# Kernel tuning notes

Measured on AMD Instinct MI355X. Metric: run time of the kernel, lower is better.

## Reference

```python
import jax, jax.numpy as jnp
import numpy as np

D = 512
H_G = 8
H_L = 8
WIN = 2
B = 4
S = 2048
LN_EPS = 1e-5


def layer_norm(x, g, b):
    m = jnp.mean(x, axis=-1, keepdims=True)
    v = jnp.mean(jnp.square(x - m), axis=-1, keepdims=True)
    return (x - m) * jax.lax.rsqrt(v + LN_EPS) * g + b


def mha(x, w_in, b_in, w_out, b_out, n_heads, mask=None):
    # x: [B', S', D]; w_in: [3D, D]; torch nn.MultiheadAttention math (eval, no dropout)
    Bp, Sp, Dm = x.shape
    dh = Dm // n_heads
    qkv = x @ w_in.T + b_in                      # [B', S', 3D]
    q, k, v = jnp.split(qkv, 3, axis=-1)
    sp = lambda t: t.reshape(Bp, Sp, n_heads, dh).transpose(0, 2, 1, 3)
    q, k, v = sp(q), sp(k), sp(v)                # [B', H, S', dh]
    scale = 1.0 / np.sqrt(dh).astype(np.float32)
    scores = jnp.einsum('bhqd,bhkd->bhqk', q, k) * scale
    if mask is not None:
        scores = scores + mask
    attn = jax.nn.softmax(scores, axis=-1)
    out = jnp.einsum('bhqk,bhkd->bhqd', attn, v)
    out = out.transpose(0, 2, 1, 3).reshape(Bp, Sp, Dm)
    return out @ w_out.T + b_out


def setup_inputs() -> dict:
    key = jax.random.key(0)
    ks = jax.random.split(key, 12)
    s = 0.02
    inp = {
        'x': jax.random.normal(ks[0], (B, S, D), jnp.float32),
        'ln1_g': jnp.ones((D,), jnp.float32), 'ln1_b': jnp.zeros((D,), jnp.float32),
        'ln2_g': jnp.ones((D,), jnp.float32), 'ln2_b': jnp.zeros((D,), jnp.float32),
        'ln3_g': jnp.ones((D,), jnp.float32), 'ln3_b': jnp.zeros((D,), jnp.float32),
        'gw_in': jax.random.normal(ks[1], (3 * D, D), jnp.float32) * s,
        'gb_in': jnp.zeros((3 * D,), jnp.float32),
        'gw_out': jax.random.normal(ks[2], (D, D), jnp.float32) * s,
        'gb_out': jnp.zeros((D,), jnp.float32),
        'lw_in': jax.random.normal(ks[3], (3 * D, D), jnp.float32) * s,
        'lb_in': jnp.zeros((3 * D,), jnp.float32),
        'lw_out': jax.random.normal(ks[4], (D, D), jnp.float32) * s,
        'lb_out': jnp.zeros((D,), jnp.float32),
        'gate_w': jax.random.normal(ks[5], (D, D), jnp.float32) * s,
        'gate_b': jnp.zeros((D,), jnp.float32),
        'ff_w1': jax.random.normal(ks[6], (4 * D, D), jnp.float32) * s,
        'ff_b1': jnp.zeros((4 * D,), jnp.float32),
        'ff_w2': jax.random.normal(ks[7], (D, 4 * D), jnp.float32) * s,
        'ff_b2': jnp.zeros((D,), jnp.float32),
    }
    return inp


def reference(x, ln1_g, ln1_b, ln2_g, ln2_b, ln3_g, ln3_b,
              gw_in, gb_in, gw_out, gb_out,
              lw_in, lb_in, lw_out, lb_out,
              gate_w, gate_b, ff_w1, ff_b1, ff_w2, ff_b2):
    Bb, Ss, Dm = x.shape
    x_norm = layer_norm(x, ln1_g, ln1_b)

    # global causal attention
    causal = jnp.triu(jnp.full((Ss, Ss), -jnp.inf, jnp.float32), 1)
    g_out = mha(x_norm, gw_in, gb_in, gw_out, gb_out, H_G, mask=causal)

    xl = x_norm.reshape(Bb * (Ss // WIN), WIN, Dm)
    l_out = mha(xl, lw_in, lb_in, lw_out, lb_out, H_L).reshape(Bb, Ss, Dm)

    gate = jax.nn.sigmoid(x_norm @ gate_w.T + gate_b)
    x = x + gate * g_out + (1.0 - gate) * l_out

    h = layer_norm(x, ln2_g, ln2_b)
    h = jax.nn.gelu(h @ ff_w1.T + ff_b1, approximate=False) @ ff_w2.T + ff_b2
    x = x + h
    return layer_norm(x, ln3_g, ln3_b)
```

## Files before the change

### kernel.cpp

```cpp
#include <hip/hip_runtime.h>
#include <math.h>
#include <stdint.h>

typedef unsigned short u16;
typedef __attribute__((ext_vector_type(4))) unsigned short u16x4;
typedef __attribute__((ext_vector_type(8))) unsigned short u16x8;
typedef __attribute__((ext_vector_type(8))) short s16x8;
typedef __attribute__((ext_vector_type(4))) float f32x4;

constexpr int Bc = 4;
constexpr int Sq = 2048;
constexpr int Dm = 512;
constexpr int Mrows = Bc * Sq;
constexpr int QW = 3072;

__device__ inline float b2f(u16 h) {
  union { uint32_t u; float f; } x; x.u = (uint32_t)h << 16; return x.f;
}
__device__ inline u16 f2bf(float f) {
  union { float f; uint32_t u; } x; x.f = f;
  uint32_t r = (x.u + 0x7fffu + ((x.u >> 16) & 1u)) >> 16;
  return (u16)r;
}

constexpr size_t W_GWIN  = 0;
constexpr size_t W_LWIN  = 786432;
constexpr size_t W_GWOUT = 1572864;
constexpr size_t W_LWOUT = 1835008;
constexpr size_t W_GATE  = 2097152;
constexpr size_t W_FF1   = 2359296;
constexpr size_t W_FF2   = 3407872;
constexpr size_t W_TOTAL = 4456448;

__global__ __launch_bounds__(256) void wconv_kernel(
    const float* __restrict__ gw_in, const float* __restrict__ lw_in,
    const float* __restrict__ gw_out, const float* __restrict__ lw_out,
    const float* __restrict__ gate_w, const float* __restrict__ ff_w1,
    const float* __restrict__ ff_w2, u16* __restrict__ dst) {
  size_t idx = ((size_t)blockIdx.x * 256 + threadIdx.x) * 4;
  if (idx >= W_TOTAL) return;
  const float* src; size_t base;
  if      (idx < W_LWIN)  { src = gw_in;  base = W_GWIN;  }
  else if (idx < W_GWOUT) { src = lw_in;  base = W_LWIN;  }
  else if (idx < W_LWOUT) { src = gw_out; base = W_GWOUT; }
  else if (idx < W_GATE)  { src = lw_out; base = W_LWOUT; }
  else if (idx < W_FF1)   { src = gate_w; base = W_GATE;  }
  else if (idx < W_FF2)   { src = ff_w1;  base = W_FF1;   }
  else                    { src = ff_w2;  base = W_FF2;   }
  float4 v = *reinterpret_cast<const float4*>(src + (idx - base));
  u16x4 o = { f2bf(v.x), f2bf(v.y), f2bf(v.z), f2bf(v.w) };
  *reinterpret_cast<u16x4*>(dst + idx) = o;
}

template <bool OB>
__global__ __launch_bounds__(128) void ln_kernel(
    const float* __restrict__ in, const float* __restrict__ add,
    const float* __restrict__ add2,
    const float* __restrict__ g, const float* __restrict__ b,
    void* __restrict__ outp) {
  const int row = blockIdx.x;
  const int t = threadIdx.x;
  float4 v = reinterpret_cast<const float4*>(in + (size_t)row * Dm)[t];
  if (add != nullptr) {
    float4 a = reinterpret_cast<const float4*>(add + (size_t)row * Dm)[t];
    v.x += a.x; v.y += a.y; v.z += a.z; v.w += a.w;
  }
  if (add2 != nullptr) {
    float4 a = reinterpret_cast<const float4*>(add2 + (size_t)row * Dm)[t];
    v.x += a.x; v.y += a.y; v.z += a.z; v.w += a.w;
  }
  float s  = v.x + v.y + v.z + v.w;
  float s2 = v.x*v.x + v.y*v.y + v.z*v.z + v.w*v.w;
  #pragma unroll
  for (int o = 32; o > 0; o >>= 1) {
    s  += __shfl_down(s, o);
    s2 += __shfl_down(s2, o);
  }
  __shared__ float rs[2], rs2[2];
  if ((t & 63) == 0) { rs[t >> 6] = s; rs2[t >> 6] = s2; }
  __syncthreads();
  const float mean = (rs[0] + rs[1]) * (1.0f / Dm);
  const float var  = (rs2[0] + rs2[1]) * (1.0f / Dm) - mean * mean;
  const float rstd = rsqrtf(var + 1e-5f);
  float4 gv = reinterpret_cast<const float4*>(g)[t];
  float4 bv = reinterpret_cast<const float4*>(b)[t];
  float ox = (v.x - mean) * rstd * gv.x + bv.x;
  float oy = (v.y - mean) * rstd * gv.y + bv.y;
  float oz = (v.z - mean) * rstd * gv.z + bv.z;
  float ow = (v.w - mean) * rstd * gv.w + bv.w;
  if (OB) {
    u16x4 o4 = { f2bf(ox), f2bf(oy), f2bf(oz), f2bf(ow) };
    *reinterpret_cast<u16x4*>((u16*)outp + (size_t)row * Dm + t * 4) = o4;
  } else {
    float4 o4; o4.x = ox; o4.y = oy; o4.z = oz; o4.w = ow;
    reinterpret_cast<float4*>((float*)outp + (size_t)row * Dm)[t] = o4;
  }
}

template <int ACT, bool OUT_BF16>
__global__ __launch_bounds__(256) void mfma_gemm(
    const u16* __restrict__ A, const u16* __restrict__ W,
    const float* __restrict__ bias, const float* __restrict__ bias2, int bsplit,
    void* __restrict__ Cout, int N, int K) {
  __shared__ u16 sA[128 * 32];
  __shared__ u16 sW[128 * 32];
  const int tid  = threadIdx.x;
  const int wid  = tid >> 6, lane = tid & 63;
  const int lr   = lane & 15, kh = lane >> 4;
  const int wm   = wid >> 1, wn = wid & 1;
  const int m0   = blockIdx.y * 128, n0 = blockIdx.x * 128;
  const int row0 = tid >> 2,        ko0 = (tid & 3) * 8;
  const int row1 = (256 + tid) >> 2, ko1 = (tid & 3) * 8;

  f32x4 acc[4][4] = {};
  for (int k0 = 0; k0 < K; k0 += 32) {
    __syncthreads();
    __builtin_amdgcn_global_load_lds(
        (const __attribute__((address_space(1))) void*)(A + (size_t)(m0 + row0) * K + k0 + ko0),
        (__attribute__((address_space(3))) void*)(sA + wid * 512), 16, 0, 0);
    __builtin_amdgcn_global_load_lds(
        (const __attribute__((address_space(1))) void*)(A + (size_t)(m0 + row1) * K + k0 + ko1),
        (__attribute__((address_space(3))) void*)(sA + 2048 + wid * 512), 16, 0, 0);
    __builtin_amdgcn_global_load_lds(
        (const __attribute__((address_space(1))) void*)(W + (size_t)(n0 + row0) * K + k0 + ko0),
        (__attribute__((address_space(3))) void*)(sW + wid * 512), 16, 0, 0);
    __builtin_amdgcn_global_load_lds(
        (const __attribute__((address_space(1))) void*)(W + (size_t)(n0 + row1) * K + k0 + ko1),
        (__attribute__((address_space(3))) void*)(sW + 2048 + wid * 512), 16, 0, 0);
    __syncthreads();
    s16x8 af[4], bf[4];
    #pragma unroll
    for (int mf = 0; mf < 4; ++mf)
      af[mf] = *reinterpret_cast<const s16x8*>(&sA[(wm * 64 + mf * 16 + lr) * 32 + kh * 8]);
    #pragma unroll
    for (int nf = 0; nf < 4; ++nf)
      bf[nf] = *reinterpret_cast<const s16x8*>(&sW[(wn * 64 + nf * 16 + lr) * 32 + kh * 8]);
    #pragma unroll
    for (int mf = 0; mf < 4; ++mf)
      #pragma unroll
      for (int nf = 0; nf < 4; ++nf)
        acc[mf][nf] = __builtin_amdgcn_mfma_f32_16x16x32_bf16(af[mf], bf[nf], acc[mf][nf], 0, 0, 0);
  }
  #pragma unroll
  for (int nf = 0; nf < 4; ++nf) {
    const int col = n0 + wn * 64 + nf * 16 + lr;
    const float bv = (bias2 != nullptr && col >= bsplit) ? bias2[col - bsplit] : bias[col];
    #pragma unroll
    for (int mf = 0; mf < 4; ++mf) {
      #pragma unroll
      for (int j = 0; j < 4; ++j) {
        const int rowg = m0 + wm * 64 + mf * 16 + kh * 4 + j;
        float v = acc[mf][nf][j] + bv;
        if (ACT == 1) v = 1.0f / (1.0f + expf(-v));
        else if (ACT == 2) v = 0.5f * v * (1.0f + erff(v * 0.70710678118654752440f));
        if (OUT_BF16) ((u16*)Cout)[(size_t)rowg * N + col] = f2bf(v);
        else          ((float*)Cout)[(size_t)rowg * N + col] = v;
      }
    }
  }
}

__global__ __launch_bounds__(256) void mfma_gemm_sk(
    const u16* __restrict__ A, const u16* __restrict__ W,
    const float* __restrict__ bias, float* __restrict__ C0, float* __restrict__ C1,
    int N, int Kt) {
  __shared__ u16 sA[128 * 32];
  __shared__ u16 sW[128 * 32];
  const int tid  = threadIdx.x;
  const int wid  = tid >> 6, lane = tid & 63;
  const int lr   = lane & 15, kh = lane >> 4;
  const int wm   = wid >> 1, wn = wid & 1;
  const int m0   = blockIdx.y * 128, n0 = blockIdx.x * 128;
  const int z    = blockIdx.z;
  const int kbeg = z * (Kt / 2), kend = kbeg + (Kt / 2);
  const int row0 = tid >> 2,        ko0 = (tid & 3) * 8;
  const int row1 = (256 + tid) >> 2, ko1 = (tid & 3) * 8;

  f32x4 acc[4][4] = {};
  for (int k0 = kbeg; k0 < kend; k0 += 32) {
    __syncthreads();
    __builtin_amdgcn_global_load_lds(
        (const __attribute__((address_space(1))) void*)(A + (size_t)(m0 + row0) * Kt + k0 + ko0),
        (__attribute__((address_space(3))) void*)(sA + wid * 512), 16, 0, 0);
    __builtin_amdgcn_global_load_lds(
        (const __attribute__((address_space(1))) void*)(A + (size_t)(m0 + row1) * Kt + k0 + ko1),
        (__attribute__((address_space(3))) void*)(sA + 2048 + wid * 512), 16, 0, 0);
    __builtin_amdgcn_global_load_lds(
        (const __attribute__((address_space(1))) void*)(W + (size_t)(n0 + row0) * Kt + k0 + ko0),
        (__attribute__((address_space(3))) void*)(sW + wid * 512), 16, 0, 0);
    __builtin_amdgcn_global_load_lds(
        (const __attribute__((address_space(1))) void*)(W + (size_t)(n0 + row1) * Kt + k0 + ko1),
        (__attribute__((address_space(3))) void*)(sW + 2048 + wid * 512), 16, 0, 0);
    __syncthreads();
    s16x8 af[4], bf[4];
    #pragma unroll
    for (int mf = 0; mf < 4; ++mf)
      af[mf] = *reinterpret_cast<const s16x8*>(&sA[(wm * 64 + mf * 16 + lr) * 32 + kh * 8]);
    #pragma unroll
    for (int nf = 0; nf < 4; ++nf)
      bf[nf] = *reinterpret_cast<const s16x8*>(&sW[(wn * 64 + nf * 16 + lr) * 32 + kh * 8]);
    #pragma unroll
    for (int mf = 0; mf < 4; ++mf)
      #pragma unroll
      for (int nf = 0; nf < 4; ++nf)
        acc[mf][nf] = __builtin_amdgcn_mfma_f32_16x16x32_bf16(af[mf], bf[nf], acc[mf][nf], 0, 0, 0);
  }
  float* C = z ? C1 : C0;
  #pragma unroll
  for (int nf = 0; nf < 4; ++nf) {
    const int col = n0 + wn * 64 + nf * 16 + lr;
    const float bv = z ? 0.0f : bias[col];
    #pragma unroll
    for (int mf = 0; mf < 4; ++mf) {
      #pragma unroll
      for (int j = 0; j < 4; ++j) {
        const int rowg = m0 + wm * 64 + mf * 16 + kh * 4 + j;
        C[(size_t)rowg * N + col] = acc[mf][nf][j] + bv;
      }
    }
  }
}

__global__ __launch_bounds__(256) void fuse3_kernel(
    const u16* __restrict__ A0, const u16* __restrict__ A1, const u16* __restrict__ A2,
    const u16* __restrict__ Wg, const u16* __restrict__ Wgo, const u16* __restrict__ Wlo,
    const float* __restrict__ bg, const float* __restrict__ bgo, const float* __restrict__ blo,
    const float* __restrict__ x, float* __restrict__ x2) {
  constexpr int N = 512, K = 512;
  __shared__ u16 sA[128 * 32];
  __shared__ u16 sW[128 * 32];
  const int tid  = threadIdx.x;
  const int wid  = tid >> 6, lane = tid & 63;
  const int lr   = lane & 15, kh = lane >> 4;
  const int wm   = wid >> 1, wn = wid & 1;
  const int m0   = blockIdx.y * 128, n0 = blockIdx.x * 128;
  const int row0 = tid >> 2,        ko0 = (tid & 3) * 8;
  const int row1 = (256 + tid) >> 2, ko1 = (tid & 3) * 8;

  f32x4 gv[4][4], pgv[4][4], acc[4][4];
  for (int pass = 0; pass < 3; ++pass) {
    const u16* A = (pass == 0) ? A0 : (pass == 1) ? A1 : A2;
    const u16* W = (pass == 0) ? Wg : (pass == 1) ? Wgo : Wlo;
    #pragma unroll
    for (int mf = 0; mf < 4; ++mf)
      #pragma unroll
      for (int nf = 0; nf < 4; ++nf)
        acc[mf][nf] = f32x4{0.f, 0.f, 0.f, 0.f};
    for (int k0 = 0; k0 < K; k0 += 32) {
      __syncthreads();
      __builtin_amdgcn_global_load_lds(
          (const __attribute__((address_space(1))) void*)(A + (size_t)(m0 + row0) * K + k0 + ko0),
          (__attribute__((address_space(3))) void*)(sA + wid * 512), 16, 0, 0);
      __builtin_amdgcn_global_load_lds(
          (const __attribute__((address_space(1))) void*)(A + (size_t)(m0 + row1) * K + k0 + ko1),
          (__attribute__((address_space(3))) void*)(sA + 2048 + wid * 512), 16, 0, 0);
      __builtin_amdgcn_global_load_lds(
          (const __attribute__((address_space(1))) void*)(W + (size_t)(n0 + row0) * K + k0 + ko0),
          (__attribute__((address_space(3))) void*)(sW + wid * 512), 16, 0, 0);
      __builtin_amdgcn_global_load_lds(
          (const __attribute__((address_space(1))) void*)(W + (size_t)(n0 + row1) * K + k0 + ko1),
          (__attribute__((address_space(3))) void*)(sW + 2048 + wid * 512), 16, 0, 0);
      __syncthreads();
      s16x8 af[4], bf[4];
      #pragma unroll
      for (int mf = 0; mf < 4; ++mf)
        af[mf] = *reinterpret_cast<const s16x8*>(&sA[(wm * 64 + mf * 16 + lr) * 32 + kh * 8]);
      #pragma unroll
      for (int nf = 0; nf < 4; ++nf)
        bf[nf] = *reinterpret_cast<const s16x8*>(&sW[(wn * 64 + nf * 16 + lr) * 32 + kh * 8]);
      #pragma unroll
      for (int mf = 0; mf < 4; ++mf)
        #pragma unroll
        for (int nf = 0; nf < 4; ++nf)
          acc[mf][nf] = __builtin_amdgcn_mfma_f32_16x16x32_bf16(af[mf], bf[nf], acc[mf][nf], 0, 0, 0);
    }
    if (pass == 0) {
      #pragma unroll
      for (int nf = 0; nf < 4; ++nf) {
        const float bv = bg[n0 + wn * 64 + nf * 16 + lr];
        #pragma unroll
        for (int mf = 0; mf < 4; ++mf)
          #pragma unroll
          for (int j = 0; j < 4; ++j)
            gv[mf][nf][j] = 1.0f / (1.0f + __expf(-(acc[mf][nf][j] + bv)));
      }
    } else if (pass == 1) {
      #pragma unroll
      for (int nf = 0; nf < 4; ++nf) {
        const float bv = bgo[n0 + wn * 64 + nf * 16 + lr];
        #pragma unroll
        for (int mf = 0; mf < 4; ++mf)
          #pragma unroll
          for (int j = 0; j < 4; ++j)
            pgv[mf][nf][j] = acc[mf][nf][j] + bv;
      }
    }
  }
  #pragma unroll
  for (int nf = 0; nf < 4; ++nf) {
    const int col = n0 + wn * 64 + nf * 16 + lr;
    const float bv = blo[col];
    #pragma unroll
    for (int mf = 0; mf < 4; ++mf) {
      #pragma unroll
      for (int j = 0; j < 4; ++j) {
        const int rowg = m0 + wm * 64 + mf * 16 + kh * 4 + j;
        const float pl = acc[mf][nf][j] + bv;
        const float g  = gv[mf][nf][j];
        const float pg = pgv[mf][nf][j];
        x2[(size_t)rowg * N + col] = x[(size_t)rowg * N + col] + g * pg + (1.0f - g) * pl;
      }
    }
  }
}

__global__ __launch_bounds__(256) void attn_global_kernel(
    const u16* __restrict__ qkv, u16* __restrict__ outb,
    float* __restrict__ opart, float* __restrict__ ml) {
  const int id = 79 - (int)blockIdx.x;
  int qt, s, ns;
  if (id < 8)       { qt = id;                s = 0;            ns = 1; }
  else if (id < 24) { int t = id - 8;  qt = 8 + (t >> 1);  s = t & 1;  ns = 2; }
  else if (id < 48) { int t = id - 24; int q3 = t / 3; qt = 16 + q3; s = t - q3 * 3; ns = 3; }
  else              { int t = id - 48; qt = 24 + (t >> 2); s = t & 3;  ns = 4; }
  const int kt0 = s * 8;
  const int kt1 = min(kt0 + 8, qt + 1);

  const int h  = blockIdx.y;
  const int b  = blockIdx.z;
  const int tid = threadIdx.x;
  const int w = tid >> 6, lane = tid & 63;
  const int c = lane & 15, kh = lane >> 4;
  constexpr float TS = 0.125f * 1.44269504088896f;

  __shared__ u16 Kb[64][72];
  __shared__ u16 Vt[64][72];
  __shared__ u16 Pw[4][16][72];

  const size_t bbase = (size_t)b * Sq;

  s16x8 aq[2];
  {
    const u16* qg = qkv + (bbase + qt * 64 + w * 16 + c) * QW + h * 64 + kh * 8;
    aq[0] = *reinterpret_cast<const s16x8*>(qg);
    aq[1] = *reinterpret_cast<const s16x8*>(qg + 32);
  }

  f32x4 o_acc[4] = {};
  float mrow[4] = { -INFINITY, -INFINITY, -INFINITY, -INFINITY };
  float lrow[4] = { 0.f, 0.f, 0.f, 0.f };
  int qp[4];
  #pragma unroll
  for (int j = 0; j < 4; ++j) qp[j] = qt * 64 + w * 16 + kh * 4 + j;

  const int g2 = tid >> 3, cc = tid & 7;
  const int srow2 = g2 * 2;
  const u16* kg0 = qkv + (bbase + srow2) * QW + 512 + h * 64 + cc * 8;
  const size_t tilestep = (size_t)64 * QW;

  u16x8 ka, kb2, va, vb;
  {
    const u16* p = kg0 + (size_t)kt0 * tilestep;
    ka  = *reinterpret_cast<const u16x8*>(p);
    kb2 = *reinterpret_cast<const u16x8*>(p + QW);
    va  = *reinterpret_cast<const u16x8*>(p + 512);
    vb  = *reinterpret_cast<const u16x8*>(p + QW + 512);
  }

  for (int kt = kt0; kt < kt1; ++kt) {
    __syncthreads();
    {
      *reinterpret_cast<u16x8*>(&Kb[srow2][cc * 8])     = ka;
      *reinterpret_cast<u16x8*>(&Kb[srow2 + 1][cc * 8]) = kb2;
      const int sw = srow2 ^ (cc * 8);
      #pragma unroll
      for (int i = 0; i < 8; ++i) {
        uint32_t pk = (uint32_t)va[i] | ((uint32_t)vb[i] << 16);
        *reinterpret_cast<uint32_t*>(&Vt[cc * 8 + i][sw]) = pk;
      }
    }
    __syncthreads();
    if (kt + 1 < kt1) {
      const u16* p = kg0 + (size_t)(kt + 1) * tilestep;
      ka  = *reinterpret_cast<const u16x8*>(p);
      kb2 = *reinterpret_cast<const u16x8*>(p + QW);
      va  = *reinterpret_cast<const u16x8*>(p + 512);
      vb  = *reinterpret_cast<const u16x8*>(p + QW + 512);
    }

    f32x4 s_acc[4] = {};
    #pragma unroll
    for (int nb = 0; nb < 4; ++nb) {
      #pragma unroll
      for (int kk = 0; kk < 2; ++kk) {
        s16x8 bk = *reinterpret_cast<const s16x8*>(&Kb[nb * 16 + c][kk * 32 + kh * 8]);
        s_acc[nb] = __builtin_amdgcn_mfma_f32_16x16x32_bf16(aq[kk], bk, s_acc[nb], 0, 0, 0);
      }
    }

    const bool diag = (kt == qt);
    float p[4][4];
    float tm[4] = { -INFINITY, -INFINITY, -INFINITY, -INFINITY };
    #pragma unroll
    for (int nb = 0; nb < 4; ++nb) {
      #pragma unroll
      for (int j = 0; j < 4; ++j) {
        float sv = s_acc[nb][j] * TS;
        if (diag && (kt * 64 + nb * 16 + c) > qp[j]) sv = -INFINITY;
        p[nb][j] = sv;
        tm[j] = fmaxf(tm[j], sv);
      }
    }
    #pragma unroll
    for (int o = 1; o < 16; o <<= 1) {
      #pragma unroll
      for (int j = 0; j < 4; ++j) tm[j] = fmaxf(tm[j], __shfl_xor(tm[j], o));
    }
    #pragma unroll
    for (int j = 0; j < 4; ++j) {
      const float mnew = fmaxf(mrow[j], tm[j]);
      const float corr = exp2f(mrow[j] - mnew);
      mrow[j] = mnew;
      float ps = 0.f;
      #pragma unroll
      for (int nb = 0; nb < 4; ++nb) {
        p[nb][j] = exp2f(p[nb][j] - mnew);
        ps += p[nb][j];
      }
      lrow[j] = lrow[j] * corr + ps;
      #pragma unroll
      for (int nb2 = 0; nb2 < 4; ++nb2) o_acc[nb2][j] *= corr;
    }

    #pragma unroll
    for (int nb = 0; nb < 4; ++nb)
      #pragma unroll
      for (int j = 0; j < 4; ++j)
        Pw[w][kh * 4 + j][nb * 16 + c] = f2bf(p[nb][j]);

    #pragma unroll
    for (int kk = 0; kk < 2; ++kk) {
      s16x8 ap = *reinterpret_cast<const s16x8*>(&Pw[w][c][kk * 32 + kh * 8]);
      #pragma unroll
      for (int nb2 = 0; nb2 < 4; ++nb2) {
        const int dh = nb2 * 16 + c;
        const int f8 = ((dh >> 3) & 7) * 8;
        s16x8 bv = *reinterpret_cast<const s16x8*>(&Vt[dh][(kk * 32 + kh * 8) ^ f8]);
        o_acc[nb2] = __builtin_amdgcn_mfma_f32_16x16x32_bf16(ap, bv, o_acc[nb2], 0, 0, 0);
      }
    }
  }

  #pragma unroll
  for (int o = 1; o < 16; o <<= 1) {
    #pragma unroll
    for (int j = 0; j < 4; ++j) lrow[j] += __shfl_xor(lrow[j], o);
  }

  if (ns == 1) {
    float invl[4];
    #pragma unroll
    for (int j = 0; j < 4; ++j) invl[j] = 1.0f / lrow[j];
    #pragma unroll
    for (int nb2 = 0; nb2 < 4; ++nb2)
      #pragma unroll
      for (int j = 0; j < 4; ++j) {
        const int qrow = qt * 64 + w * 16 + kh * 4 + j;
        outb[(bbase + qrow) * Dm + h * 64 + nb2 * 16 + c] = f2bf(o_acc[nb2][j] * invl[j]);
      }
  } else {
    const size_t pid = (size_t)(b * 8 + h) * 72 + (id - 8);
    float* op = opart + pid * 4096;
    #pragma unroll
    for (int nb2 = 0; nb2 < 4; ++nb2)
      #pragma unroll
      for (int j = 0; j < 4; ++j)
        op[(w * 16 + kh * 4 + j) * 64 + nb2 * 16 + c] = o_acc[nb2][j];
    if (c == 0) {
      #pragma unroll
      for (int j = 0; j < 4; ++j) {
        ml[pid * 128 + w * 16 + kh * 4 + j]      = mrow[j];
        ml[pid * 128 + 64 + w * 16 + kh * 4 + j] = lrow[j];
      }
    }
  }
}

__global__ __launch_bounds__(256) void attn_combine_kernel(
    const float* __restrict__ opart, const float* __restrict__ ml,
    u16* __restrict__ outb) {
  const int qt = 8 + (int)blockIdx.x;
  const int h = blockIdx.y, b = blockIdx.z;
  int ns, idb;
  if (qt < 16)      { ns = 2; idb = (qt - 8) * 2; }
  else if (qt < 24) { ns = 3; idb = 16 + (qt - 16) * 3; }
  else              { ns = 4; idb = 40 + (qt - 24) * 4; }
  const int r  = threadIdx.x >> 2;
  const int d0 = (threadIdx.x & 3) * 16;
  const size_t pidb = (size_t)(b * 8 + h) * 72 + idb;

  float M = -INFINITY;
  for (int s2 = 0; s2 < ns; ++s2)
    M = fmaxf(M, ml[(pidb + s2) * 128 + r]);
  float L = 0.f;
  f32x4 o0 = {}, o1 = {}, o2 = {}, o3 = {};
  for (int s2 = 0; s2 < ns; ++s2) {
    const size_t pp = pidb + s2;
    const float wgt = exp2f(ml[pp * 128 + r] - M);
    L += wgt * ml[pp * 128 + 64 + r];
    const float* op = opart + pp * 4096 + (size_t)r * 64 + d0;
    f32x4 a0 = *reinterpret_cast<const f32x4*>(op);
    f32x4 a1 = *reinterpret_cast<const f32x4*>(op + 4);
    f32x4 a2 = *reinterpret_cast<const f32x4*>(op + 8);
    f32x4 a3 = *reinterpret_cast<const f32x4*>(op + 12);
    #pragma unroll
    for (int i = 0; i < 4; ++i) {
      o0[i] += wgt * a0[i]; o1[i] += wgt * a1[i];
      o2[i] += wgt * a2[i]; o3[i] += wgt * a3[i];
    }
  }
  const float invL = 1.0f / L;
  u16* dst = outb + ((size_t)b * Sq + qt * 64 + r) * Dm + h * 64 + d0;
  u16x4 w0 = { f2bf(o0[0]*invL), f2bf(o0[1]*invL), f2bf(o0[2]*invL), f2bf(o0[3]*invL) };
  u16x4 w1 = { f2bf(o1[0]*invL), f2bf(o1[1]*invL), f2bf(o1[2]*invL), f2bf(o1[3]*invL) };
  u16x4 w2 = { f2bf(o2[0]*invL), f2bf(o2[1]*invL), f2bf(o2[2]*invL), f2bf(o2[3]*invL) };
  u16x4 w3 = { f2bf(o3[0]*invL), f2bf(o3[1]*invL), f2bf(o3[2]*invL), f2bf(o3[3]*invL) };
  *reinterpret_cast<u16x4*>(dst)      = w0;
  *reinterpret_cast<u16x4*>(dst + 4)  = w1;
  *reinterpret_cast<u16x4*>(dst + 8)  = w2;
  *reinterpret_cast<u16x4*>(dst + 12) = w3;
}

__global__ __launch_bounds__(256) void attn_local_kernel(
    const u16* __restrict__ qkv, u16* __restrict__ outb) {
  const int unit = blockIdx.x * 4 + (threadIdx.x >> 6);
  const int lane = threadIdx.x & 63;
  const int h = unit & 7;
  const size_t pair = (size_t)(unit >> 3);
  const u16* r0 = qkv + pair * 2 * QW + 1536;
  const u16* r1 = r0 + QW;
  const int off = h * 64 + lane;
  const float q0 = b2f(r0[off]), k0 = b2f(r0[512 + off]), v0 = b2f(r0[1024 + off]);
  const float q1 = b2f(r1[off]), k1 = b2f(r1[512 + off]), v1 = b2f(r1[1024 + off]);
  float s00 = q0 * k0, s01 = q0 * k1, s10 = q1 * k0, s11 = q1 * k1;
  #pragma unroll
  for (int o = 1; o < 64; o <<= 1) {
    s00 += __shfl_xor(s00, o); s01 += __shfl_xor(s01, o);
    s10 += __shfl_xor(s10, o); s11 += __shfl_xor(s11, o);
  }
  s00 *= 0.125f; s01 *= 0.125f; s10 *= 0.125f; s11 *= 0.125f;
  const float m0 = fmaxf(s00, s01), m1 = fmaxf(s10, s11);
  const float e00 = expf(s00 - m0), e01 = expf(s01 - m0);
  const float e10 = expf(s10 - m1), e11 = expf(s11 - m1);
  const float w0 = 1.0f / (e00 + e01), w1 = 1.0f / (e10 + e11);
  outb[pair * 2 * Dm + off]       = f2bf((e00 * v0 + e01 * v1) * w0);
  outb[(pair * 2 + 1) * Dm + off] = f2bf((e10 * v0 + e11 * v1) * w1);
}

extern "C" void kernel_launch(void* const* d_in, const int* in_sizes, int n_in,
                              void* d_out, int out_size, void* d_ws, size_t ws_size,
                              hipStream_t stream) {
  const float* x      = (const float*)d_in[0];
  const float* ln1_g  = (const float*)d_in[1];
  const float* ln1_b  = (const float*)d_in[2];
  const float* ln2_g  = (const float*)d_in[3];
  const float* ln2_b  = (const float*)d_in[4];
  const float* ln3_g  = (const float*)d_in[5];
  const float* ln3_b  = (const float*)d_in[6];
  const float* gw_in  = (const float*)d_in[7];
  const float* gb_in  = (const float*)d_in[8];
  const float* gw_out = (const float*)d_in[9];
  const float* gb_out = (const float*)d_in[10];
  const float* lw_in  = (const float*)d_in[11];
  const float* lb_in  = (const float*)d_in[12];
  const float* lw_out = (const float*)d_in[13];
  const float* lb_out = (const float*)d_in[14];
  const float* gate_w = (const float*)d_in[15];
  const float* gate_b = (const float*)d_in[16];
  const float* ff_w1  = (const float*)d_in[17];
  const float* ff_b1  = (const float*)d_in[18];
  const float* ff_w2  = (const float*)d_in[19];
  const float* ff_b2  = (const float*)d_in[20];
  float* out = (float*)d_out;
  char* wsb  = (char*)d_ws;

  u16*   xnb   = (u16*)(wsb + 0);
  u16*   qkvb  = (u16*)(wsb + 8388608);
  u16*   ff1b  = qkvb;
  float* h2b   = (float*)(wsb + 41943040);
  u16*   attgb = (u16*)(wsb + 58720256);
  u16*   attlb = (u16*)(wsb + 67108864);
  u16*   wb    = (u16*)(wsb + 75497472);
  float* opart = (float*)(wsb + 84410368);
  float* ml    = (float*)(wsb + 122159104);
  float* x2    = (float*)(wsb + 84410368);
  float* h2a   = (float*)(wsb + 101187584);

  wconv_kernel<<<(W_TOTAL / 4 + 255) / 256, 256, 0, stream>>>(
      gw_in, lw_in, gw_out, lw_out, gate_w, ff_w1, ff_w2, wb);
  ln_kernel<true><<<Mrows, 128, 0, stream>>>(x, nullptr, nullptr, ln1_g, ln1_b, xnb);
  mfma_gemm<0, true><<<dim3(QW / 128, Mrows / 128), 256, 0, stream>>>(
      xnb, wb, gb_in, lb_in, 1536, qkvb, QW, 512);
  attn_local_kernel<<<(Mrows / 2) * 8 / 4, 256, 0, stream>>>(qkvb, attlb);
  attn_global_kernel<<<dim3(80, 8, Bc), 256, 0, stream>>>(qkvb, attgb, opart, ml);
  attn_combine_kernel<<<dim3(24, 8, Bc), 256, 0, stream>>>(opart, ml, attgb);
  fuse3_kernel<<<dim3(512 / 128, Mrows / 128), 256, 0, stream>>>(
      xnb, attgb, attlb, wb + W_GATE, wb + W_GWOUT, wb + W_LWOUT,
      gate_b, gb_out, lb_out, x, x2);
  ln_kernel<true><<<Mrows, 128, 0, stream>>>(x2, nullptr, nullptr, ln2_g, ln2_b, xnb);
  mfma_gemm<2, true><<<dim3(2048 / 128, Mrows / 128), 256, 0, stream>>>(
      xnb, wb + W_FF1, ff_b1, nullptr, 0, ff1b, 2048, 512);
  mfma_gemm_sk<<<dim3(512 / 128, Mrows / 128, 2), 256, 0, stream>>>(
      ff1b, wb + W_FF2, ff_b2, h2a, h2b, 512, 2048);
  ln_kernel<false><<<Mrows, 128, 0, stream>>>(x2, h2a, h2b, ln3_g, ln3_b, out);
}
```

Measured before the change: 280.2 us.

## Run gate and local-out GEMMs inside global attention launch to fill idle CUs

The QKV GEMM now writes the global and local QKV into two separate compact buffers. The gate and local out-projection GEMMs move out of the fused epilogue kernel and run as extra blocks of the global attention launch, so they overlap with the unevenly loaded causal attention blocks. The epilogue kernel now does only the global out-projection and reads the gate and local projection back from bf16 buffers. This adds extra memory round trips and bf16 rounding of the gate. It also makes two smaller changes: P is truncated rather than rounded to bf16, and the causal mask is applied only on the diagonal tile.

```diff
diff --git a/kernel.cpp b/kernel.cpp
--- a/kernel.cpp
+++ b/kernel.cpp
@@ -12,7 +12,6 @@
 constexpr int Sq = 2048;
 constexpr int Dm = 512;
 constexpr int Mrows = Bc * Sq;
-constexpr int QW = 3072;
 
 __device__ inline float b2f(u16 h) {
   union { uint32_t u; float f; } x; x.u = (uint32_t)h << 16; return x.f;
@@ -97,11 +96,11 @@
   }
 }
 
-template <int ACT, bool OUT_BF16>
+template <int ACT, bool OUT_BF16, bool SPLITQ>
 __global__ __launch_bounds__(256) void mfma_gemm(
     const u16* __restrict__ A, const u16* __restrict__ W,
     const float* __restrict__ bias, const float* __restrict__ bias2, int bsplit,
-    void* __restrict__ Cout, int N, int K) {
+    void* __restrict__ Cout, void* __restrict__ Cout2, int N, int K) {
   __shared__ u16 sA[128 * 32];
   __shared__ u16 sW[128 * 32];
   const int tid  = threadIdx.x;
@@ -153,8 +152,15 @@
         float v = acc[mf][nf][j] + bv;
         if (ACT == 1) v = 1.0f / (1.0f + expf(-v));
         else if (ACT == 2) v = 0.5f * v * (1.0f + erff(v * 0.70710678118654752440f));
-        if (OUT_BF16) ((u16*)Cout)[(size_t)rowg * N + col] = f2bf(v);
-        else          ((float*)Cout)[(size_t)rowg * N + col] = v;
+        if (SPLITQ) {
+          u16* dst = (col < bsplit) ? (u16*)Cout : (u16*)Cout2;
+          const int cc = (col < bsplit) ? col : col - bsplit;
+          dst[(size_t)rowg * bsplit + cc] = f2bf(v);
+        } else if (OUT_BF16) {
+          ((u16*)Cout)[(size_t)rowg * N + col] = f2bf(v);
+        } else {
+          ((float*)Cout)[(size_t)rowg * N + col] = v;
+        }
       }
     }
   }
@@ -221,10 +227,10 @@
   }
 }
 
-__global__ __launch_bounds__(256) void fuse3_kernel(
-    const u16* __restrict__ A0, const u16* __restrict__ A1, const u16* __restrict__ A2,
-    const u16* __restrict__ Wg, const u16* __restrict__ Wgo, const u16* __restrict__ Wlo,
-    const float* __restrict__ bg, const float* __restrict__ bgo, const float* __restrict__ blo,
+__global__ __launch_bounds__(256) void fuse1_kernel(
+    const u16* __restrict__ A, const u16* __restrict__ W,
+    const float* __restrict__ bgo,
+    const u16* __restrict__ gateb, const u16* __restrict__ plb,
     const float* __restrict__ x, float* __restrict__ x2) {
   constexpr int N = 512, K = 512;
   __shared__ u16 sA[128 * 32];
@@ -237,15 +243,88 @@
   const int row0 = tid >> 2,        ko0 = (tid & 3) * 8;
   const int row1 = (256 + tid) >> 2, ko1 = (tid & 3) * 8;
 
-  f32x4 gv[4][4], pgv[4][4], acc[4][4];
-  for (int pass = 0; pass < 3; ++pass) {
-    const u16* A = (pass == 0) ? A0 : (pass == 1) ? A1 : A2;
-    const u16* W = (pass == 0) ? Wg : (pass == 1) ? Wgo : Wlo;
+  f32x4 acc[4][4] = {};
+  for (int k0 = 0; k0 < K; k0 += 32) {
+    __syncthreads();
+    __builtin_amdgcn_global_load_lds(
+        (const __attribute__((address_space(1))) void*)(A + (size_t)(m0 + row0) * K + k0 + ko0),
+        (__attribute__((address_space(3))) void*)(sA + wid * 512), 16, 0, 0);
+    __builtin_amdgcn_global_load_lds(
+        (const __attribute__((address_space(1))) void*)(A + (size_t)(m0 + row1) * K + k0 + ko1),
+        (__attribute__((address_space(3))) void*)(sA + 2048 + wid * 512), 16, 0, 0);
+    __builtin_amdgcn_global_load_lds(
+        (const __attribute__((address_space(1))) void*)(W + (size_t)(n0 + row0) * K + k0 + ko0),
+        (__attribute__((address_space(3))) void*)(sW + wid * 512), 16, 0, 0);
+    __builtin_amdgcn_global_load_lds(
+        (const __attribute__((address_space(1))) void*)(W + (size_t)(n0 + row1) * K + k0 + ko1),
+        (__attribute__((address_space(3))) void*)(sW + 2048 + wid * 512), 16, 0, 0);
+    __syncthreads();
+    s16x8 af[4], bf[4];
     #pragma unroll
     for (int mf = 0; mf < 4; ++mf)
+      af[mf] = *reinterpret_cast<const s16x8*>(&sA[(wm * 64 + mf * 16 + lr) * 32 + kh * 8]);
+    #pragma unroll
+    for (int nf = 0; nf < 4; ++nf)
+      bf[nf] = *reinterpret_cast<const s16x8*>(&sW[(wn * 64 + nf * 16 + lr) * 32 + kh * 8]);
+    #pragma unroll
+    for (int mf = 0; mf < 4; ++mf)
       #pragma unroll
       for (int nf = 0; nf < 4; ++nf)
-        acc[mf][nf] = f32x4{0.f, 0.f, 0.f, 0.f};
+        acc[mf][nf] = __builtin_amdgcn_mfma_f32_16x16x32_bf16(af[mf], bf[nf], acc[mf][nf], 0, 0, 0);
+  }
+  #pragma unroll
+  for (int nf = 0; nf < 4; ++nf) {
+    const int col = n0 + wn * 64 + nf * 16 + lr;
+    const float bv = bgo[col];
+    #pragma unroll
+    for (int mf = 0; mf < 4; ++mf) {
+      #pragma unroll
+      for (int j = 0; j < 4; ++j) {
+        const int rowg = m0 + wm * 64 + mf * 16 + kh * 4 + j;
+        const size_t off = (size_t)rowg * N + col;
+        const float pg = acc[mf][nf][j] + bv;
+        const float g  = b2f(gateb[off]);
+        const float pl = b2f(plb[off]);
+        x2[off] = x[off] + g * pg + (1.0f - g) * pl;
+      }
+    }
+  }
+}
+
+__global__ __launch_bounds__(256, 5) void attn_fat_kernel(
+    const u16* __restrict__ qkv, u16* __restrict__ outb,
+    float* __restrict__ opart, float* __restrict__ ml,
+    const u16* __restrict__ xnb, const u16* __restrict__ attlb,
+    const u16* __restrict__ Wg, const u16* __restrict__ Wlo,
+    const float* __restrict__ bg, const float* __restrict__ blo,
+    u16* __restrict__ gateb, u16* __restrict__ plb) {
+  __shared__ u16 Kb[64][72];
+  __shared__ u16 Vt[64][72];
+  __shared__ u16 Pw[4][16][72];
+
+  const int bx = blockIdx.x;
+  const int h  = blockIdx.y;
+  const int b  = blockIdx.z;
+  const int tid = threadIdx.x;
+
+  if (bx >= 80) {
+    const bool isGate = bx < 88;
+    const int lin = (bx - (isGate ? 80 : 88)) * 32 + h * 4 + b;
+    const int n0 = (lin >> 6) * 128;
+    const int m0 = (lin & 63) * 128;
+    const u16* A = isGate ? xnb : attlb;
+    const u16* W = isGate ? Wg : Wlo;
+    const float* bias = isGate ? bg : blo;
+    u16* Cout = isGate ? gateb : plb;
+    u16* sA = &Kb[0][0];
+    u16* sW = &Vt[0][0];
+    constexpr int K = 512;
+    const int wid = tid >> 6, lane = tid & 63;
+    const int lr = lane & 15, kh = lane >> 4;
+    const int wm = wid >> 1, wn = wid & 1;
+    const int row0 = tid >> 2,        ko0 = (tid & 3) * 8;
+    const int row1 = (256 + tid) >> 2, ko1 = (tid & 3) * 8;
+    f32x4 acc[4][4] = {};
     for (int k0 = 0; k0 < K; k0 += 32) {
       __syncthreads();
       __builtin_amdgcn_global_load_lds(
@@ -274,50 +353,25 @@
         for (int nf = 0; nf < 4; ++nf)
           acc[mf][nf] = __builtin_amdgcn_mfma_f32_16x16x32_bf16(af[mf], bf[nf], acc[mf][nf], 0, 0, 0);
     }
-    if (pass == 0) {
-      #pragma unroll
-      for (int nf = 0; nf < 4; ++nf) {
-        const float bv = bg[n0 + wn * 64 + nf * 16 + lr];
+    #pragma unroll
+    for (int nf = 0; nf < 4; ++nf) {
+      const int col = n0 + wn * 64 + nf * 16 + lr;
+      const float bv = bias[col];
+      #pragma unroll
+      for (int mf = 0; mf < 4; ++mf) {
         #pragma unroll
-        for (int mf = 0; mf < 4; ++mf)
-          #pragma unroll
-          for (int j = 0; j < 4; ++j)
-            gv[mf][nf][j] = 1.0f / (1.0f + __expf(-(acc[mf][nf][j] + bv)));
-      }
-    } else if (pass == 1) {
-      #pragma unroll
-      for (int nf = 0; nf < 4; ++nf) {
-        const float bv = bgo[n0 + wn * 64 + nf * 16 + lr];
-        #pragma unroll
-        for (int mf = 0; mf < 4; ++mf)
-          #pragma unroll
-          for (int j = 0; j < 4; ++j)
-            pgv[mf][nf][j] = acc[mf][nf][j] + bv;
-      }
-    }
-  }
-  #pragma unroll
-  for (int nf = 0; nf < 4; ++nf) {
-    const int col = n0 + wn * 64 + nf * 16 + lr;
-    const float bv = blo[col];
-    #pragma unroll
-    for (int mf = 0; mf < 4; ++mf) {
-      #pragma unroll
-      for (int j = 0; j < 4; ++j) {
-        const int rowg = m0 + wm * 64 + mf * 16 + kh * 4 + j;
-        const float pl = acc[mf][nf][j] + bv;
-        const float g  = gv[mf][nf][j];
-        const float pg = pgv[mf][nf][j];
-        x2[(size_t)rowg * N + col] = x[(size_t)rowg * N + col] + g * pg + (1.0f - g) * pl;
-      }
-    }
-  }
-}
-
-__global__ __launch_bounds__(256) void attn_global_kernel(
-    const u16* __restrict__ qkv, u16* __restrict__ outb,
-    float* __restrict__ opart, float* __restrict__ ml) {
-  const int id = 79 - (int)blockIdx.x;
+        for (int j = 0; j < 4; ++j) {
+          const int rowg = m0 + wm * 64 + mf * 16 + kh * 4 + j;
+          float v = acc[mf][nf][j] + bv;
+          if (isGate) v = 1.0f / (1.0f + __expf(-v));
+          Cout[(size_t)rowg * 512 + col] = f2bf(v);
+        }
+      }
+    }
+    return;
+  }
+
+  const int id = 79 - bx;
   int qt, s, ns;
   if (id < 8)       { qt = id;                s = 0;            ns = 1; }
   else if (id < 24) { int t = id - 8;  qt = 8 + (t >> 1);  s = t & 1;  ns = 2; }
@@ -326,22 +380,15 @@
   const int kt0 = s * 8;
   const int kt1 = min(kt0 + 8, qt + 1);
 
-  const int h  = blockIdx.y;
-  const int b  = blockIdx.z;
-  const int tid = threadIdx.x;
   const int w = tid >> 6, lane = tid & 63;
   const int c = lane & 15, kh = lane >> 4;
   constexpr float TS = 0.125f * 1.44269504088896f;
 
-  __shared__ u16 Kb[64][72];
-  __shared__ u16 Vt[64][72];
-  __shared__ u16 Pw[4][16][72];
-
   const size_t bbase = (size_t)b * Sq;
 
   s16x8 aq[2];
   {
-    const u16* qg = qkv + (bbase + qt * 64 + w * 16 + c) * QW + h * 64 + kh * 8;
+    const u16* qg = qkv + (bbase + qt * 64 + w * 16 + c) * 1536 + h * 64 + kh * 8;
     aq[0] = *reinterpret_cast<const s16x8*>(qg);
     aq[1] = *reinterpret_cast<const s16x8*>(qg + 32);
   }
@@ -349,22 +396,20 @@
   f32x4 o_acc[4] = {};
   float mrow[4] = { -INFINITY, -INFINITY, -INFINITY, -INFINITY };
   float lrow[4] = { 0.f, 0.f, 0.f, 0.f };
-  int qp[4];
-  #pragma unroll
-  for (int j = 0; j < 4; ++j) qp[j] = qt * 64 + w * 16 + kh * 4 + j;
+  const int qbase = qt * 64 + w * 16 + kh * 4;
 
   const int g2 = tid >> 3, cc = tid & 7;
   const int srow2 = g2 * 2;
-  const u16* kg0 = qkv + (bbase + srow2) * QW + 512 + h * 64 + cc * 8;
-  const size_t tilestep = (size_t)64 * QW;
+  const u16* kg0 = qkv + (bbase + srow2) * 1536 + 512 + h * 64 + cc * 8;
+  const size_t tilestep = (size_t)64 * 1536;
 
   u16x8 ka, kb2, va, vb;
   {
     const u16* p = kg0 + (size_t)kt0 * tilestep;
     ka  = *reinterpret_cast<const u16x8*>(p);
-    kb2 = *reinterpret_cast<const u16x8*>(p + QW);
+    kb2 = *reinterpret_cast<const u16x8*>(p + 1536);
     va  = *reinterpret_cast<const u16x8*>(p + 512);
-    vb  = *reinterpret_cast<const u16x8*>(p + QW + 512);
+    vb  = *reinterpret_cast<const u16x8*>(p + 1536 + 512);
   }
 
   for (int kt = kt0; kt < kt1; ++kt) {
@@ -383,9 +428,9 @@
     if (kt + 1 < kt1) {
       const u16* p = kg0 + (size_t)(kt + 1) * tilestep;
       ka  = *reinterpret_cast<const u16x8*>(p);
-      kb2 = *reinterpret_cast<const u16x8*>(p + QW);
+      kb2 = *reinterpret_cast<const u16x8*>(p + 1536);
       va  = *reinterpret_cast<const u16x8*>(p + 512);
-      vb  = *reinterpret_cast<const u16x8*>(p + QW + 512);
+      vb  = *reinterpret_cast<const u16x8*>(p + 1536 + 512);
     }
 
     f32x4 s_acc[4] = {};
@@ -398,19 +443,25 @@
       }
     }
 
-    const bool diag = (kt == qt);
     float p[4][4];
-    float tm[4] = { -INFINITY, -INFINITY, -INFINITY, -INFINITY };
-    #pragma unroll
-    for (int nb = 0; nb < 4; ++nb) {
-      #pragma unroll
-      for (int j = 0; j < 4; ++j) {
-        float sv = s_acc[nb][j] * TS;
-        if (diag && (kt * 64 + nb * 16 + c) > qp[j]) sv = -INFINITY;
-        p[nb][j] = sv;
-        tm[j] = fmaxf(tm[j], sv);
-      }
-    }
+    #pragma unroll
+    for (int nb = 0; nb < 4; ++nb)
+      #pragma unroll
+      for (int j = 0; j < 4; ++j)
+        p[nb][j] = s_acc[nb][j] * TS;
+    if (kt == qt) {
+      #pragma unroll
+      for (int nb = 0; nb < 4; ++nb) {
+        const int kp = kt * 64 + nb * 16 + c;
+        #pragma unroll
+        for (int j = 0; j < 4; ++j)
+          if (kp > qbase + j) p[nb][j] = -INFINITY;
+      }
+    }
+    float tm[4];
+    #pragma unroll
+    for (int j = 0; j < 4; ++j)
+      tm[j] = fmaxf(fmaxf(p[0][j], p[1][j]), fmaxf(p[2][j], p[3][j]));
     #pragma unroll
     for (int o = 1; o < 16; o <<= 1) {
       #pragma unroll
@@ -436,7 +487,7 @@
     for (int nb = 0; nb < 4; ++nb)
       #pragma unroll
       for (int j = 0; j < 4; ++j)
-        Pw[w][kh * 4 + j][nb * 16 + c] = f2bf(p[nb][j]);
+        Pw[w][kh * 4 + j][nb * 16 + c] = (u16)(__float_as_uint(p[nb][j]) >> 16);
 
     #pragma unroll
     for (int kk = 0; kk < 2; ++kk) {
@@ -532,13 +583,13 @@
 }
 
 __global__ __launch_bounds__(256) void attn_local_kernel(
-    const u16* __restrict__ qkv, u16* __restrict__ outb) {
+    const u16* __restrict__ qkvl, u16* __restrict__ outb) {
   const int unit = blockIdx.x * 4 + (threadIdx.x >> 6);
   const int lane = threadIdx.x & 63;
   const int h = unit & 7;
   const size_t pair = (size_t)(unit >> 3);
-  const u16* r0 = qkv + pair * 2 * QW + 1536;
-  const u16* r1 = r0 + QW;
+  const u16* r0 = qkvl + pair * 2 * 1536;
+  const u16* r1 = r0 + 1536;
   const int off = h * 64 + lane;
   const float q0 = b2f(r0[off]), k0 = b2f(r0[512 + off]), v0 = b2f(r0[1024 + off]);
   const float q1 = b2f(r1[off]), k1 = b2f(r1[512 + off]), v1 = b2f(r1[1024 + off]);
@@ -585,9 +636,10 @@
   char* wsb  = (char*)d_ws;
 
   u16*   xnb   = (u16*)(wsb + 0);
-  u16*   qkvb  = (u16*)(wsb + 8388608);
-  u16*   ff1b  = qkvb;
-  float* h2b   = (float*)(wsb + 41943040);
+  u16*   qkvg  = (u16*)(wsb + 8388608);
+  u16*   qkvl  = (u16*)(wsb + 33554432);
+  u16*   gateb = (u16*)(wsb + 33554432);
+  u16*   plb   = (u16*)(wsb + 41943040);
   u16*   attgb = (u16*)(wsb + 58720256);
   u16*   attlb = (u16*)(wsb + 67108864);
   u16*   wb    = (u16*)(wsb + 75497472);
@@ -595,21 +647,24 @@
   float* ml    = (float*)(wsb + 122159104);
   float* x2    = (float*)(wsb + 84410368);
   float* h2a   = (float*)(wsb + 101187584);
+  float* h2b   = (float*)(wsb + 41943040);
+  u16*   ff1b  = (u16*)(wsb + 8388608);
 
   wconv_kernel<<<(W_TOTAL / 4 + 255) / 256, 256, 0, stream>>>(
       gw_in, lw_in, gw_out, lw_out, gate_w, ff_w1, ff_w2, wb);
   ln_kernel<true><<<Mrows, 128, 0, stream>>>(x, nullptr, nullptr, ln1_g, ln1_b, xnb);
-  mfma_gemm<0, true><<<dim3(QW / 128, Mrows / 128), 256, 0, stream>>>(
-      xnb, wb, gb_in, lb_in, 1536, qkvb, QW, 512);
-  attn_local_kernel<<<(Mrows / 2) * 8 / 4, 256, 0, stream>>>(qkvb, attlb);
-  attn_global_kernel<<<dim3(80, 8, Bc), 256, 0, stream>>>(qkvb, attgb, opart, ml);
+  mfma_gemm<0, true, true><<<dim3(3072 / 128, Mrows / 128), 256, 0, stream>>>(
+      xnb, wb, gb_in, lb_in, 1536, qkvg, qkvl, 3072, 512);
+  attn_local_kernel<<<(Mrows / 2) * 8 / 4, 256, 0, stream>>>(qkvl, attlb);
+  attn_fat_kernel<<<dim3(96, 8, Bc), 256, 0, stream>>>(
+      qkvg, attgb, opart, ml, xnb, attlb,
+      wb + W_GATE, wb + W_LWOUT, gate_b, lb_out, gateb, plb);
   attn_combine_kernel<<<dim3(24, 8, Bc), 256, 0, stream>>>(opart, ml, attgb);
-  fuse3_kernel<<<dim3(512 / 128, Mrows / 128), 256, 0, stream>>>(
-      xnb, attgb, attlb, wb + W_GATE, wb + W_GWOUT, wb + W_LWOUT,
-      gate_b, gb_out, lb_out, x, x2);
+  fuse1_kernel<<<dim3(512 / 128, Mrows / 128), 256, 0, stream>>>(
+      attgb, wb + W_GWOUT, gb_out, gateb, plb, x, x2);
   ln_kernel<true><<<Mrows, 128, 0, stream>>>(x2, nullptr, nullptr, ln2_g, ln2_b, xnb);
-  mfma_gemm<2, true><<<dim3(2048 / 128, Mrows / 128), 256, 0, stream>>>(
-      xnb, wb + W_FF1, ff_b1, nullptr, 0, ff1b, 2048, 512);
+  mfma_gemm<2, true, false><<<dim3(2048 / 128, Mrows / 128), 256, 0, stream>>>(
+      xnb, wb + W_FF1, ff_b1, nullptr, 0, ff1b, nullptr, 2048, 512);
   mfma_gemm_sk<<<dim3(512 / 128, Mrows / 128, 2), 256, 0, stream>>>(
       ff1b, wb + W_FF2, ff_b2, h2a, h2b, 512, 2048);
   ln_kernel<false><<<Mrows, 128, 0, stream>>>(x2, h2a, h2b, ln3_g, ln3_b, out);
```

After: 278.6 us. Within noise of the previous version (-0.6%).
